# Performance work log

Measured on AMD Instinct MI355X. Metric: run time of the kernel, lower is better.

Reference implementation:

```python
import jax, jax.numpy as jnp
import numpy as np

MATRIX_SIZE = 16  # dims = 256 = 16**2
N_POINTS = 16384
N_TIMES = 512
OMEGA_ZERO = 2.0


def _block_diag_generator(m):
    # block_diag of [[0,1],[-1,0]] * (i+1) for i in range(m//2)
    A = np.zeros((m, m), dtype=np.float32)
    for i in range(m // 2):
        s = (i + 1.0)
        A[2 * i, 2 * i + 1] = s
        A[2 * i + 1, 2 * i] = -s
    return jnp.asarray(A)


def setup_inputs() -> dict:
    key = jax.random.key(0)
    k1, k2 = jax.random.split(key)
    x = jax.random.normal(k1, (N_POINTS, MATRIX_SIZE), dtype=jnp.float32)
    t = jax.random.uniform(k2, (N_TIMES,), dtype=jnp.float32)
    omega = OMEGA_ZERO * jnp.ones((1,), dtype=jnp.float32)  # nn.Parameter init
    M = _block_diag_generator(MATRIX_SIZE)                  # buffer
    M0 = jnp.zeros((MATRIX_SIZE, MATRIX_SIZE), dtype=jnp.float32)  # buffer (default)
    return {"x": x, "t": t, "omega": omega, "M": M, "M0": M0}


def reference(x, t, omega, M, M0):
    # A = (M * omega + M0) scaled per-time: (T, m, m)
    A = (M * omega[0] + M0)[None, :, :] * t[:, None, None]
    A_ex = jax.vmap(jax.scipy.linalg.expm)(A)  # batched matrix exponential (T, m, m)
    # x: (N, m); torch does (T,m,m) @ (1,m,N) -> (T,m,N), then transpose -> (T,N,m)
    out = jnp.einsum('tij,nj->tni', A_ex, x)
    return out
```

## Files before the change

kernel.cpp:

```cpp
#include <hip/hip_runtime.h>


#define MDIM 16
#define MELEMS 256
#define RPT 8
#define ROWS_PER_BLOCK 512

__global__ __launch_bounds__(256) void expm_kernel(
    const float* __restrict__ t,
    const float* __restrict__ omega,
    const float* __restrict__ M,
    const float* __restrict__ M0,
    float* __restrict__ E ) {
  __shared__ float A[MELEMS];
  __shared__ float T[MELEMS];
  __shared__ float rowsum[MDIM];

  const int bt  = blockIdx.x;
  const int tid = threadIdx.x;
  const int i = tid >> 4;
  const int j = tid & 15;

  const float tv = t[bt];
  const float om = omega[0];
  const float a = (M[tid] * om + M0[tid]) * tv;

  float rs = fabsf(a);
  rs += __shfl_xor(rs, 1);
  rs += __shfl_xor(rs, 2);
  rs += __shfl_xor(rs, 4);
  rs += __shfl_xor(rs, 8);
  if (j == 0) rowsum[i] = rs;
  __syncthreads();
  float nrm = 0.f;
#pragma unroll
  for (int r = 0; r < MDIM; ++r) nrm = fmaxf(nrm, rowsum[r]);
  int s = 0;
  while (nrm > 0.5f && s < 40) { nrm *= 0.5f; ++s; }

  const float b = ldexpf(a, -s);
  const float ident = (i == j) ? 1.0f : 0.0f;
  A[tid] = b;
  T[tid] = ident;
  __syncthreads();

  for (int k = 12; k >= 1; --k) {
    float acc = 0.f;
#pragma unroll
    for (int c = 0; c < MDIM; ++c) acc += A[i * MDIM + c] * T[c * MDIM + j];
    __syncthreads();
    T[tid] = ident + acc * (1.0f / (float)k);
    __syncthreads();
  }

  for (int k = 0; k < s; ++k) {
    float acc = 0.f;
#pragma unroll
    for (int c = 0; c < MDIM; ++c) acc += T[i * MDIM + c] * T[c * MDIM + j];
    __syncthreads();
    T[tid] = acc;
    __syncthreads();
  }

  E[(size_t)bt * MELEMS + tid] = T[tid];
}

__global__ __launch_bounds__(256) void apply_kernel(
    const float* __restrict__ E,
    const float* __restrict__ x,
    float* __restrict__ out,
    int N) {
  __shared__ __align__(16) float Es[MDIM * 20];
  const int t   = blockIdx.y;
  const int tid = threadIdx.x;
  {
    const int r = tid >> 4, c = tid & 15;
    Es[r * 20 + c] = E[(size_t)t * MELEMS + tid];
  }
  __syncthreads();

  const int i4 = tid & 3;
  const int nl = tid >> 2;

  float4 e[16];
#pragma unroll
  for (int k = 0; k < 4; ++k) {
    const float* row = Es + (i4 * 4 + k) * 20;
#pragma unroll
    for (int q = 0; q < 4; ++q) e[k * 4 + q] = *(const float4*)(row + q * 4);
  }

  const size_t nb = (size_t)blockIdx.x * ROWS_PER_BLOCK;
  const float4* __restrict__ xin = (const float4*)x;
  float4* __restrict__ op = (float4*)(out + ((size_t)t * N + nb) * MDIM);

#pragma unroll
  for (int k = 0; k < RPT; ++k) {
    const size_t n = nb + nl + (size_t)k * 64;
    const float4 x0 = xin[n * 4 + 0];
    const float4 x1 = xin[n * 4 + 1];
    const float4 x2 = xin[n * 4 + 2];
    const float4 x3 = xin[n * 4 + 3];

    float o[4];
#pragma unroll
    for (int r = 0; r < 4; ++r) {
      const float4 e0 = e[r * 4 + 0], e1 = e[r * 4 + 1];
      const float4 e2 = e[r * 4 + 2], e3 = e[r * 4 + 3];
      o[r] = e0.x * x0.x + e0.y * x0.y + e0.z * x0.z + e0.w * x0.w
           + e1.x * x1.x + e1.y * x1.y + e1.z * x1.z + e1.w * x1.w
           + e2.x * x2.x + e2.y * x2.y + e2.z * x2.z + e2.w * x2.w
           + e3.x * x3.x + e3.y * x3.y + e3.z * x3.z + e3.w * x3.w;
    }
    op[k * 256 + tid] = make_float4(o[0], o[1], o[2], o[3]);
  }
}

extern "C" void kernel_launch(void* const* d_in, const int* in_sizes, int n_in,
                              void* d_out, int out_size, void* d_ws, size_t ws_size,
                              hipStream_t stream) {
  const float* x     = (const float*)d_in[0];
  const float* t     = (const float*)d_in[1];
  const float* omega = (const float*)d_in[2];
  const float* M     = (const float*)d_in[3];
  const float* M0    = (const float*)d_in[4];
  float* out = (float*)d_out;

  const int N = in_sizes[0] / MDIM;
  const int T = in_sizes[1];

  float* E = (float*)d_ws;

  expm_kernel<<<T, 256, 0, stream>>>(t, omega, M, M0, E);

  dim3 grid(N / ROWS_PER_BLOCK, T);
  apply_kernel<<<grid, 256, 0, stream>>>(E, x, out, N);
}
```

Before: 127.0 us.

## Cut Taylor order, compute scaling exponent directly, double-buffer x loads

The expm kernel now finds the scaling exponent with ilogbf instead of a halving loop, and drops the Taylor series from 12 to 8 terms. This adds one squaring step in exchange for fewer series multiplications, and may change accuracy slightly. The apply kernel ping-pongs between two register sets of x, so the next rows load while the current ones are computed, and it sets launch_bounds to a minimum of 4 blocks. The apply kernel writes 512x16384x16 floats and is bound by memory writes, so the software pipelining likely changes little.

New measurement: 117.1 us. 1.08x faster.

```diff
diff --git a/kernel.cpp b/kernel.cpp
--- a/kernel.cpp
+++ b/kernel.cpp
@@ -1,4 +1,5 @@
 #include <hip/hip_runtime.h>
+#include <math.h>
 
 
 #define MDIM 16
@@ -35,8 +36,8 @@
   float nrm = 0.f;
 #pragma unroll
   for (int r = 0; r < MDIM; ++r) nrm = fmaxf(nrm, rowsum[r]);
-  int s = 0;
-  while (nrm > 0.5f && s < 40) { nrm *= 0.5f; ++s; }
+  int s = (nrm > 1e-30f) ? (ilogbf(nrm) + 2) : 0;
+  if (s < 0) s = 0;
 
   const float b = ldexpf(a, -s);
   const float ident = (i == j) ? 1.0f : 0.0f;
@@ -44,7 +45,7 @@
   T[tid] = ident;
   __syncthreads();
 
-  for (int k = 12; k >= 1; --k) {
+  for (int k = 8; k >= 1; --k) {
     float acc = 0.f;
 #pragma unroll
     for (int c = 0; c < MDIM; ++c) acc += A[i * MDIM + c] * T[c * MDIM + j];
@@ -65,7 +66,7 @@
   E[(size_t)bt * MELEMS + tid] = T[tid];
 }
 
-__global__ __launch_bounds__(256) void apply_kernel(
+__global__ __launch_bounds__(256, 4) void apply_kernel(
     const float* __restrict__ E,
     const float* __restrict__ x,
     float* __restrict__ out,
@@ -94,26 +95,39 @@
   const float4* __restrict__ xin = (const float4*)x;
   float4* __restrict__ op = (float4*)(out + ((size_t)t * N + nb) * MDIM);
 
+  float4 xa0, xa1, xa2, xa3, xb0, xb1, xb2, xb3;
+
+#define LOADX(d0, d1, d2, d3, k) do {                         \
+    const size_t base = (nb + nl + (size_t)(k) * 64) * 4;     \
+    d0 = xin[base + 0]; d1 = xin[base + 1];                   \
+    d2 = xin[base + 2]; d3 = xin[base + 3];                   \
+  } while (0)
+
+#define DOT(o, x0, x1, x2, x3) do {                                        \
+    _Pragma("unroll")                                                      \
+    for (int r = 0; r < 4; ++r) {                                          \
+      const float4 e0 = e[r * 4 + 0], e1 = e[r * 4 + 1];                   \
+      const float4 e2 = e[r * 4 + 2], e3 = e[r * 4 + 3];                   \
+      o[r] = e0.x * x0.x + e0.y * x0.y + e0.z * x0.z + e0.w * x0.w         \
+           + e1.x * x1.x + e1.y * x1.y + e1.z * x1.z + e1.w * x1.w         \
+           + e2.x * x2.x + e2.y * x2.y + e2.z * x2.z + e2.w * x2.w         \
+           + e3.x * x3.x + e3.y * x3.y + e3.z * x3.z + e3.w * x3.w;        \
+    }                                                                      \
+  } while (0)
+
+  LOADX(xa0, xa1, xa2, xa3, 0);
 #pragma unroll
-  for (int k = 0; k < RPT; ++k) {
-    const size_t n = nb + nl + (size_t)k * 64;
-    const float4 x0 = xin[n * 4 + 0];
-    const float4 x1 = xin[n * 4 + 1];
-    const float4 x2 = xin[n * 4 + 2];
-    const float4 x3 = xin[n * 4 + 3];
-
+  for (int k = 0; k < RPT; k += 2) {
     float o[4];
-#pragma unroll
-    for (int r = 0; r < 4; ++r) {
-      const float4 e0 = e[r * 4 + 0], e1 = e[r * 4 + 1];
-      const float4 e2 = e[r * 4 + 2], e3 = e[r * 4 + 3];
-      o[r] = e0.x * x0.x + e0.y * x0.y + e0.z * x0.z + e0.w * x0.w
-           + e1.x * x1.x + e1.y * x1.y + e1.z * x1.z + e1.w * x1.w
-           + e2.x * x2.x + e2.y * x2.y + e2.z * x2.z + e2.w * x2.w
-           + e3.x * x3.x + e3.y * x3.y + e3.z * x3.z + e3.w * x3.w;
-    }
+    if (k + 1 < RPT) LOADX(xb0, xb1, xb2, xb3, k + 1);
+    DOT(o, xa0, xa1, xa2, xa3);
     op[k * 256 + tid] = make_float4(o[0], o[1], o[2], o[3]);
+    if (k + 2 < RPT) LOADX(xa0, xa1, xa2, xa3, k + 2);
+    DOT(o, xb0, xb1, xb2, xb3);
+    op[(k + 1) * 256 + tid] = make_float4(o[0], o[1], o[2], o[3]);
   }
+#undef LOADX
+#undef DOT
 }
 
 extern "C" void kernel_launch(void* const* d_in, const int* in_sizes, int n_in,
```

## Keep x rows in registers and loop over times with scalar E loads

Applied to the files above, without the earlier changes.

The apply kernel is restructured so each thread keeps one row of x in registers and loops over 128 time steps. Each wave computes 4 output columns, reading E through wave-uniform addresses that can become scalar loads, which removes the shared-memory staging and the repeated x reloads per time step. The expm kernel now gets its scaling exponent from ilogbf instead of a loop and drops the Taylor degree from 12 to 8 terms, which cuts compute but may slightly lower accuracy. Each wave stores only 16 bytes per row with a large stride between rows, so output writes are less contiguous than before.

After: 213.2 us. +68.0%, slower.

```diff
diff --git a/kernel.cpp b/kernel.cpp
--- a/kernel.cpp
+++ b/kernel.cpp
@@ -1,10 +1,12 @@
 #include <hip/hip_runtime.h>
+#include <math.h>
 
 
 #define MDIM 16
 #define MELEMS 256
-#define RPT 8
-#define ROWS_PER_BLOCK 512
+#define T_PER_BLOCK 128
+
+typedef float f32x4 __attribute__((ext_vector_type(4)));
 
 __global__ __launch_bounds__(256) void expm_kernel(
     const float* __restrict__ t,
@@ -35,8 +37,8 @@
   float nrm = 0.f;
 #pragma unroll
   for (int r = 0; r < MDIM; ++r) nrm = fmaxf(nrm, rowsum[r]);
-  int s = 0;
-  while (nrm > 0.5f && s < 40) { nrm *= 0.5f; ++s; }
+  int s = (nrm > 1e-30f) ? (ilogbf(nrm) + 2) : 0;
+  if (s < 0) s = 0;
 
   const float b = ldexpf(a, -s);
   const float ident = (i == j) ? 1.0f : 0.0f;
@@ -44,7 +46,7 @@
   T[tid] = ident;
   __syncthreads();
 
-  for (int k = 12; k >= 1; --k) {
+  for (int k = 8; k >= 1; --k) {
     float acc = 0.f;
 #pragma unroll
     for (int c = 0; c < MDIM; ++c) acc += A[i * MDIM + c] * T[c * MDIM + j];
@@ -70,49 +72,44 @@
     const float* __restrict__ x,
     float* __restrict__ out,
     int N) {
-  __shared__ __align__(16) float Es[MDIM * 20];
-  const int t   = blockIdx.y;
-  const int tid = threadIdx.x;
+  const int rgn  = N >> 6;
+  const int bx   = blockIdx.x;
+  const int rg   = bx % rgn;
+  const int tq   = bx / rgn;
+  const int lane = threadIdx.x & 63;
+  const int w    = __builtin_amdgcn_readfirstlane(threadIdx.x >> 6);
+  const int row  = rg * 64 + lane;
+
+  float xr[MDIM];
   {
-    const int r = tid >> 4, c = tid & 15;
-    Es[r * 20 + c] = E[(size_t)t * MELEMS + tid];
-  }
-  __syncthreads();
-
-  const int i4 = tid & 3;
-  const int nl = tid >> 2;
-
-  float4 e[16];
+    const f32x4* xrow = (const f32x4*)(x + (size_t)row * MDIM);
 #pragma unroll
-  for (int k = 0; k < 4; ++k) {
-    const float* row = Es + (i4 * 4 + k) * 20;
-#pragma unroll
-    for (int q = 0; q < 4; ++q) e[k * 4 + q] = *(const float4*)(row + q * 4);
+    for (int q = 0; q < 4; ++q) {
+      const f32x4 v = xrow[q];
+      xr[q * 4 + 0] = v.x; xr[q * 4 + 1] = v.y;
+      xr[q * 4 + 2] = v.z; xr[q * 4 + 3] = v.w;
+    }
   }
 
-  const size_t nb = (size_t)blockIdx.x * ROWS_PER_BLOCK;
-  const float4* __restrict__ xin = (const float4*)x;
-  float4* __restrict__ op = (float4*)(out + ((size_t)t * N + nb) * MDIM);
+  const int t0 = tq * T_PER_BLOCK;
+  const float* __restrict__ Ew = E + (size_t)w * 64;
+  float* __restrict__ ob = out + (size_t)row * MDIM + (size_t)w * 4;
 
-#pragma unroll
-  for (int k = 0; k < RPT; ++k) {
-    const size_t n = nb + nl + (size_t)k * 64;
-    const float4 x0 = xin[n * 4 + 0];
-    const float4 x1 = xin[n * 4 + 1];
-    const float4 x2 = xin[n * 4 + 2];
-    const float4 x3 = xin[n * 4 + 3];
-
+#pragma unroll 4
+  for (int tt = 0; tt < T_PER_BLOCK; ++tt) {
+    const int t = t0 + tt;
+    const float* __restrict__ Eb = Ew + (size_t)t * MELEMS;
     float o[4];
 #pragma unroll
-    for (int r = 0; r < 4; ++r) {
-      const float4 e0 = e[r * 4 + 0], e1 = e[r * 4 + 1];
-      const float4 e2 = e[r * 4 + 2], e3 = e[r * 4 + 3];
-      o[r] = e0.x * x0.x + e0.y * x0.y + e0.z * x0.z + e0.w * x0.w
-           + e1.x * x1.x + e1.y * x1.y + e1.z * x1.z + e1.w * x1.w
-           + e2.x * x2.x + e2.y * x2.y + e2.z * x2.z + e2.w * x2.w
-           + e3.x * x3.x + e3.y * x3.y + e3.z * x3.z + e3.w * x3.w;
+    for (int j = 0; j < 4; ++j) {
+      const float* __restrict__ Er = Eb + j * MDIM;
+      float acc = Er[0] * xr[0];
+#pragma unroll
+      for (int c = 1; c < MDIM; ++c) acc += Er[c] * xr[c];
+      o[j] = acc;
     }
-    op[k * 256 + tid] = make_float4(o[0], o[1], o[2], o[3]);
+    f32x4 v; v.x = o[0]; v.y = o[1]; v.z = o[2]; v.w = o[3];
+    *(f32x4*)(ob + (size_t)t * N * MDIM) = v;
   }
 }
 
@@ -133,6 +130,6 @@
 
   expm_kernel<<<T, 256, 0, stream>>>(t, omega, M, M0, E);
 
-  dim3 grid(N / ROWS_PER_BLOCK, T);
+  const int grid = (N >> 6) * (T / T_PER_BLOCK);
   apply_kernel<<<grid, 256, 0, stream>>>(E, x, out, N);
 }
```

## Stage x tile in LDS and reuse it across 16 time steps per block

Applied to the files above, without the earlier changes.

The apply kernel now loads a 512-row tile of x and 16 expm matrices into shared memory once, then loops over 16 time steps, so x is read from global memory once per 16 times instead of once per time. The grid shrinks from 32x512 to 1024 blocks, and each block uses about 60 KB of LDS, which reduces occupancy. The expm kernel also computes the scaling exponent with ilogbf instead of a loop and cuts the Taylor series from 12 to 8 terms. That adds one extra squaring, so accuracy relies on the tighter scaling.

New measurement: 115.8 us. 1.1x faster.

```diff
diff --git a/kernel.cpp b/kernel.cpp
--- a/kernel.cpp
+++ b/kernel.cpp
@@ -1,10 +1,14 @@
 #include <hip/hip_runtime.h>
+#include <math.h>
 
 
 #define MDIM 16
 #define MELEMS 256
-#define RPT 8
-#define ROWS_PER_BLOCK 512
+#define RROWS 512
+#define TC 16
+#define XPAD 20
+#define EPAD 20
+#define ESTRIDE (16 * EPAD)
 
 __global__ __launch_bounds__(256) void expm_kernel(
     const float* __restrict__ t,
@@ -35,8 +39,8 @@
   float nrm = 0.f;
 #pragma unroll
   for (int r = 0; r < MDIM; ++r) nrm = fmaxf(nrm, rowsum[r]);
-  int s = 0;
-  while (nrm > 0.5f && s < 40) { nrm *= 0.5f; ++s; }
+  int s = (nrm > 1e-30f) ? (ilogbf(nrm) + 2) : 0;
+  if (s < 0) s = 0;
 
   const float b = ldexpf(a, -s);
   const float ident = (i == j) ? 1.0f : 0.0f;
@@ -44,7 +48,7 @@
   T[tid] = ident;
   __syncthreads();
 
-  for (int k = 12; k >= 1; --k) {
+  for (int k = 8; k >= 1; --k) {
     float acc = 0.f;
 #pragma unroll
     for (int c = 0; c < MDIM; ++c) acc += A[i * MDIM + c] * T[c * MDIM + j];
@@ -70,49 +74,73 @@
     const float* __restrict__ x,
     float* __restrict__ out,
     int N) {
-  __shared__ __align__(16) float Es[MDIM * 20];
-  const int t   = blockIdx.y;
+  __shared__ __align__(16) float XS[RROWS * XPAD];
+  __shared__ __align__(16) float ES[TC * ESTRIDE];
+
+  const int blk = blockIdx.x;
+  const int rq  = blk & 31;
+  const int tq  = blk >> 5;
   const int tid = threadIdx.x;
+  const int i4 = tid & 3;
+  const int nl = tid >> 2;
+
+  const size_t base = (size_t)rq * RROWS;
+
   {
-    const int r = tid >> 4, c = tid & 15;
-    Es[r * 20 + c] = E[(size_t)t * MELEMS + tid];
+    const float4* __restrict__ xg = (const float4*)(x + base * MDIM);
+#pragma unroll
+    for (int i = 0; i < 8; ++i) {
+      const int g = tid + i * 256;
+      const float4 v = xg[g];
+      const int row = g >> 2, ch = g & 3;
+      *(float4*)(&XS[row * XPAD + ch * 4]) = v;
+    }
+    const float4* __restrict__ eg = (const float4*)(E + (size_t)(tq * TC) * MELEMS);
+#pragma unroll
+    for (int i = 0; i < 4; ++i) {
+      const int g = tid + i * 256;
+      const float4 v = eg[g];
+      const int tl = g >> 6, rem = g & 63;
+      const int row = rem >> 2, ch = rem & 3;
+      *(float4*)(&ES[tl * ESTRIDE + row * EPAD + ch * 4]) = v;
+    }
   }
   __syncthreads();
 
-  const int i4 = tid & 3;
-  const int nl = tid >> 2;
+  const size_t slice = (size_t)N * MDIM;
 
-  float4 e[16];
+  for (int tt = 0; tt < TC; ++tt) {
+    float4 e[16];
 #pragma unroll
-  for (int k = 0; k < 4; ++k) {
-    const float* row = Es + (i4 * 4 + k) * 20;
+    for (int r = 0; r < 4; ++r)
 #pragma unroll
-    for (int q = 0; q < 4; ++q) e[k * 4 + q] = *(const float4*)(row + q * 4);
-  }
+      for (int q = 0; q < 4; ++q)
+        e[r * 4 + q] =
+            *(const float4*)(&ES[tt * ESTRIDE + (i4 * 4 + r) * EPAD + q * 4]);
 
-  const size_t nb = (size_t)blockIdx.x * ROWS_PER_BLOCK;
-  const float4* __restrict__ xin = (const float4*)x;
-  float4* __restrict__ op = (float4*)(out + ((size_t)t * N + nb) * MDIM);
+    float4* __restrict__ op =
+        (float4*)(out + (size_t)(tq * TC + tt) * slice + base * MDIM);
 
 #pragma unroll
-  for (int k = 0; k < RPT; ++k) {
-    const size_t n = nb + nl + (size_t)k * 64;
-    const float4 x0 = xin[n * 4 + 0];
-    const float4 x1 = xin[n * 4 + 1];
-    const float4 x2 = xin[n * 4 + 2];
-    const float4 x3 = xin[n * 4 + 3];
+    for (int k = 0; k < RROWS / 64; ++k) {
+      const float* __restrict__ xr = &XS[(nl + k * 64) * XPAD];
+      const float4 x0 = *(const float4*)(xr);
+      const float4 x1 = *(const float4*)(xr + 4);
+      const float4 x2 = *(const float4*)(xr + 8);
+      const float4 x3 = *(const float4*)(xr + 12);
 
-    float o[4];
+      float o[4];
 #pragma unroll
-    for (int r = 0; r < 4; ++r) {
-      const float4 e0 = e[r * 4 + 0], e1 = e[r * 4 + 1];
-      const float4 e2 = e[r * 4 + 2], e3 = e[r * 4 + 3];
-      o[r] = e0.x * x0.x + e0.y * x0.y + e0.z * x0.z + e0.w * x0.w
-           + e1.x * x1.x + e1.y * x1.y + e1.z * x1.z + e1.w * x1.w
-           + e2.x * x2.x + e2.y * x2.y + e2.z * x2.z + e2.w * x2.w
-           + e3.x * x3.x + e3.y * x3.y + e3.z * x3.z + e3.w * x3.w;
+      for (int r = 0; r < 4; ++r) {
+        const float4 ea = e[r * 4 + 0], eb = e[r * 4 + 1];
+        const float4 ec = e[r * 4 + 2], ed = e[r * 4 + 3];
+        o[r] = ea.x * x0.x + ea.y * x0.y + ea.z * x0.z + ea.w * x0.w
+             + eb.x * x1.x + eb.y * x1.y + eb.z * x1.z + eb.w * x1.w
+             + ec.x * x2.x + ec.y * x2.y + ec.z * x2.z + ec.w * x2.w
+             + ed.x * x3.x + ed.y * x3.y + ed.z * x3.z + ed.w * x3.w;
+      }
+      op[k * 256 + tid] = make_float4(o[0], o[1], o[2], o[3]);
     }
-    op[k * 256 + tid] = make_float4(o[0], o[1], o[2], o[3]);
   }
 }
 
@@ -133,6 +161,6 @@
 
   expm_kernel<<<T, 256, 0, stream>>>(t, omega, M, M0, E);
 
-  dim3 grid(N / ROWS_PER_BLOCK, T);
+  const int grid = (T / TC) * (N / RROWS);
   apply_kernel<<<grid, 256, 0, stream>>>(E, x, out, N);
 }
```
